# Kernel tuning notes

Hardware: AMD Instinct MI355X
Metric: run time of the kernel (lower is better)

## Reference

```python
import jax, jax.numpy as jnp
import numpy as np
from jax import lax

NUM_GROUP = 512    # G: number of FPS centers
GROUP_SIZE = 32    # M: KNN neighbors per center


def setup_inputs() -> dict:
    key = jax.random.key(0)
    xyz = jax.random.normal(key, (32, 8192, 3), dtype=jnp.float32)  # B N 3
    return {"xyz": xyz}


def _fps(xyz, num_group):
    """Iterative farthest point sampling. xyz: [B,N,3] -> idx [B,G] int32.
    Deterministic start at point 0 (matching pointnet2-style fps)."""
    B, N, _ = xyz.shape

    def step(carry, _):
        dists, last_idx = carry                       # dists: [B,N] running min sq-dist
        last = xyz[jnp.arange(B), last_idx]           # [B,3] most recent center
        d = jnp.sum((xyz - last[:, None, :]) ** 2, axis=-1)  # [B,N]
        dists = jnp.minimum(dists, d)
        nxt = jnp.argmax(dists, axis=-1).astype(jnp.int32)   # farthest point
        return (dists, nxt), nxt

    init_idx = jnp.zeros((B,), jnp.int32)
    init_d = jnp.full((B, N), jnp.inf, xyz.dtype)
    (_, _), idxs = lax.scan(step, (init_d, init_idx), None, length=num_group - 1)
    return jnp.concatenate([init_idx[None, :], idxs], axis=0).T  # [B,G]


def reference(xyz):
    B, N, _ = xyz.shape
    G, M = NUM_GROUP, GROUP_SIZE

    fps_idx = _fps(xyz, G)                              # [B,G] int32
    center = xyz[jnp.arange(B)[:, None], fps_idx]       # [B,G,3]

    # KNN: for each center, k nearest points in xyz (squared euclidean)
    # dist2[b,g,n] = |c|^2 + |x|^2 - 2 c.x   -> [B,G,N]
    x2 = jnp.sum(xyz * xyz, axis=-1)                    # [B,N]
    c2 = jnp.sum(center * center, axis=-1)              # [B,G]
    dist2 = c2[:, :, None] + x2[:, None, :] - 2.0 * jnp.einsum('bgd,bnd->bgn', center, xyz)
    _, idx = lax.top_k(-dist2, M)                       # [B,G,M] nearest-first

    neighborhood = xyz[jnp.arange(B)[:, None, None], idx]   # [B,G,M,3]
    neighborhood = neighborhood - center[:, :, None, :]
    return neighborhood, center, fps_idx
```

## Files before the change

kernel.cpp:

```cpp
#include <hip/hip_runtime.h>
#include <math.h>

#define BATCH  32
#define NPTS   8192
#define NGROUP 512
#define MSIZE  32

#define FPS_THREADS 512
#define SXYZ_FLOATS (NPTS * 3)
#define DYN_LDS_BYTES (SXYZ_FLOATS * 4)

#define NBLOCKS      256
#define WORKER_BLKS  (NBLOCKS - BATCH)
#define WORKER_WAVES (WORKER_BLKS * 8)
#define WPB          (WORKER_WAVES / BATCH)
#define PROG_STRIDE  16

typedef float v2f __attribute__((ext_vector_type(2)));

template<int CTRL>
__device__ __forceinline__ float dpp_max_f32(float x) {
    int o = __builtin_amdgcn_update_dpp(0, __float_as_int(x), CTRL, 0xF, 0xF, true);
    float f = __int_as_float(o);
    return x > f ? x : f;
}
template<int CTRL>
__device__ __forceinline__ unsigned dpp_min_u32_full(unsigned x) {
    unsigned o = (unsigned)__builtin_amdgcn_update_dpp(0, (int)x, CTRL, 0xF, 0xF, true);
    return o < x ? o : x;
}

__device__ __forceinline__ void fps_body(const float* __restrict__ xyz,
                                         float* __restrict__ out_center,
                                         float* __restrict__ out_fps,
                                         unsigned* __restrict__ prog,
                                         float* sxyz)
{
#pragma clang fp contract(off)
    __shared__ unsigned long long gkey[3];

    const int b    = blockIdx.x;
    const int t    = threadIdx.x;
    const int lane = t & 63;
    const float* bp = xyz + (size_t)b * NPTS * 3;
    const float4* bp4 = reinterpret_cast<const float4*>(bp);
    float4* s4 = reinterpret_cast<float4*>(sxyz);

    v2f px2[8], py2[8], pz2[8], dist2[8];
    {
        float f[48];
        #pragma unroll
        for (int q = 0; q < 12; ++q) {
            float4 v = bp4[t * 12 + q];
            s4[t * 12 + q] = v;
            f[q*4+0] = v.x; f[q*4+1] = v.y; f[q*4+2] = v.z; f[q*4+3] = v.w;
        }
        #pragma unroll
        for (int j = 0; j < 8; ++j) {
            px2[j] = (v2f){f[6*j+0], f[6*j+3]};
            py2[j] = (v2f){f[6*j+1], f[6*j+4]};
            pz2[j] = (v2f){f[6*j+2], f[6*j+5]};
            dist2[j] = (v2f){INFINITY, INFINITY};
        }
    }
    if (t == 0) { gkey[0] = 0; gkey[1] = 0; gkey[2] = 0; }
    __syncthreads();

    if (t == 0) {
        out_fps[(size_t)b * NGROUP] = 0.0f;
        __hip_atomic_store(&out_center[(size_t)(b*NGROUP)*3 + 0], sxyz[0],
                           __ATOMIC_RELAXED, __HIP_MEMORY_SCOPE_AGENT);
        __hip_atomic_store(&out_center[(size_t)(b*NGROUP)*3 + 1], sxyz[1],
                           __ATOMIC_RELAXED, __HIP_MEMORY_SCOPE_AGENT);
        __hip_atomic_store(&out_center[(size_t)(b*NGROUP)*3 + 2], sxyz[2],
                           __ATOMIC_RELAXED, __HIP_MEMORY_SCOPE_AGENT);
    }

    int last = 0;
    for (int g = 1; g < NGROUP; ++g) {
        const int slot = g % 3;
        const int nxt  = (g + 1) % 3;
        float lx = sxyz[last*3 + 0];
        float ly = sxyz[last*3 + 1];
        float lz = sxyz[last*3 + 2];

        #pragma unroll
        for (int j = 0; j < 8; ++j) {
            v2f dx = px2[j] - lx;
            v2f dy = py2[j] - ly;
            v2f dz = pz2[j] - lz;
            v2f t1 = dx * dx;
            v2f t2 = dy * dy;
            v2f t3 = dz * dz;
            v2f s  = t1 + t2;
            v2f d  = s + t3;
            dist2[j] = __builtin_elementwise_min(dist2[j], d);
        }
        v2f mm0 = __builtin_elementwise_max(dist2[0], dist2[1]);
        v2f mm1 = __builtin_elementwise_max(dist2[2], dist2[3]);
        v2f mm2 = __builtin_elementwise_max(dist2[4], dist2[5]);
        v2f mm3 = __builtin_elementwise_max(dist2[6], dist2[7]);
        v2f mma = __builtin_elementwise_max(mm0, mm1);
        v2f mmb = __builtin_elementwise_max(mm2, mm3);
        v2f mmc = __builtin_elementwise_max(mma, mmb);
        float m_t = fmaxf(mmc.x, mmc.y);

        float m = m_t;
        m = dpp_max_f32<0xB1>(m);
        m = dpp_max_f32<0x4E>(m);
        m = dpp_max_f32<0x141>(m);
        m = dpp_max_f32<0x140>(m);
        m = dpp_max_f32<0x142>(m);
        m = dpp_max_f32<0x143>(m);
        float wmax = __int_as_float(__builtin_amdgcn_readlane(__float_as_int(m), 63));

        unsigned long long mask = __ballot(m_t == wmax);
        int l = __ffsll((long long)mask) - 1;

        unsigned lj = 0;
        #pragma unroll
        for (int j = 15; j >= 0; --j) {
            float dj = (j & 1) ? dist2[j >> 1].y : dist2[j >> 1].x;
            lj = (dj == wmax) ? (unsigned)j : lj;
        }
        unsigned idx = ((unsigned)t << 4) | lj;
        unsigned widx = (unsigned)__builtin_amdgcn_readlane((int)idx, l);

        if (lane == 63) {
            unsigned long long key =
                (((unsigned long long)__float_as_uint(wmax)) << 32) | (unsigned)~widx;
            atomicMax(&gkey[slot], key);
            if (t == 63) gkey[nxt] = 0;
        }
        __syncthreads();

        unsigned long long kq = gkey[slot];
        int fi = (int)(~(unsigned)kq);
        last = fi;
        if (t == 0) {
            out_fps[(size_t)b * NGROUP + g] = (float)fi;
            const size_t o3 = ((size_t)(b * NGROUP + g)) * 3;
            __hip_atomic_store(&out_center[o3 + 0], sxyz[fi*3 + 0],
                               __ATOMIC_RELAXED, __HIP_MEMORY_SCOPE_AGENT);
            __hip_atomic_store(&out_center[o3 + 1], sxyz[fi*3 + 1],
                               __ATOMIC_RELAXED, __HIP_MEMORY_SCOPE_AGENT);
            __hip_atomic_store(&out_center[o3 + 2], sxyz[fi*3 + 2],
                               __ATOMIC_RELAXED, __HIP_MEMORY_SCOPE_AGENT);
            if ((g & 7) == 7)
                __hip_atomic_store(&prog[b * PROG_STRIDE], (unsigned)(g + 1),
                                   __ATOMIC_RELEASE, __HIP_MEMORY_SCOPE_AGENT);
        }
    }
}

__device__ __forceinline__ void knn_one_group(const float* __restrict__ bp,
                                              const float4* __restrict__ bp4,
                                              int gid, int lane,
                                              float cx, float cy, float cz,
                                              float* __restrict__ out_nbhd)
{
    unsigned kl[4];
    #pragma unroll
    for (int k = 0; k < 4; ++k) kl[k] = 0xFFFFFFFFu;

    for (int c = 0; c < 32; ++c) {
        int f4 = c * 192 + lane * 3;
        float4 a  = bp4[f4+0];
        float4 bq = bp4[f4+1];
        float4 cq = bp4[f4+2];
        unsigned p0 = (unsigned)(c * 256 + lane * 4);
        v2f xA = (v2f){a.x,  a.w},  yA = (v2f){a.y,  bq.x}, zA = (v2f){a.z,  bq.y};
        v2f xB = (v2f){bq.z, cq.y}, yB = (v2f){bq.w, cq.z}, zB = (v2f){cq.x, cq.w};
        v2f dxA = xA - cx, dyA = yA - cy, dzA = zA - cz;
        v2f dxB = xB - cx, dyB = yB - cy, dzB = zB - cz;
        v2f dA = dxA*dxA + dyA*dyA + dzA*dzA;
        v2f dB = dxB*dxB + dyB*dyB + dzB*dzB;
        float ds[4] = {dA.x, dA.y, dB.x, dB.y};
        #pragma unroll
        for (int k = 0; k < 4; ++k) {
            unsigned key = (__float_as_uint(ds[k]) & 0xFFFFE000u) | (p0 + k);
            if (key < kl[3]) {
                kl[3] = key;
                #pragma unroll
                for (int q = 3; q > 0; --q) {
                    if (kl[q] < kl[q-1]) {
                        unsigned tk = kl[q]; kl[q] = kl[q-1]; kl[q-1] = tk;
                    }
                }
            }
        }
    }

    int keep = 0;
    #pragma unroll 1
    for (int r = 0; r < MSIZE; ++r) {
        unsigned k = kl[0];
        k = dpp_min_u32_full<0xB1>(k);
        k = dpp_min_u32_full<0x4E>(k);
        k = dpp_min_u32_full<0x141>(k);
        k = dpp_min_u32_full<0x140>(k);
        {
            unsigned o = __shfl_xor(k, 16);
            k = o < k ? o : k;
            o = __shfl_xor(k, 32);
            k = o < k ? o : k;
        }
        if (lane == r) keep = (int)(k & 0x1FFFu);
        if (kl[0] == k) {
            kl[0] = kl[1]; kl[1] = kl[2]; kl[2] = kl[3];
            kl[3] = 0xFFFFFFFFu;
        }
    }

    if (lane < MSIZE) {
        size_t o = ((size_t)gid * MSIZE + lane) * 3;
        float x = bp[keep*3+0], y = bp[keep*3+1], z = bp[keep*3+2];
        out_nbhd[o+0] = x - cx;
        out_nbhd[o+1] = y - cy;
        out_nbhd[o+2] = z - cz;
    }
}

__global__ __launch_bounds__(FPS_THREADS, 2)
void fused_kernel(const float* __restrict__ xyz,
                  float* __restrict__ out_center,
                  float* __restrict__ out_fps,
                  float* __restrict__ out_nbhd,
                  unsigned* __restrict__ prog)
{
    extern __shared__ float sxyz[];

    if (blockIdx.x < BATCH) {
        fps_body(xyz, out_center, out_fps, prog, sxyz);
        return;
    }

    const int t    = threadIdx.x;
    const int lane = t & 63;
    const int wid  = t >> 6;
    const int ww   = (blockIdx.x - BATCH) * 8 + wid;
    const int b    = ww & 31;
    const int g0   = ww >> 5;
    const float* bp = xyz + (size_t)b * NPTS * 3;
    const float4* bp4 = reinterpret_cast<const float4*>(bp);

    for (int g = g0; g < NGROUP; g += WPB) {
        while ((int)__hip_atomic_load(&prog[b * PROG_STRIDE],
                                      __ATOMIC_ACQUIRE, __HIP_MEMORY_SCOPE_AGENT) <= g)
            __builtin_amdgcn_s_sleep(8);

        const int gid = b * NGROUP + g;
        float cx = __hip_atomic_load(&out_center[(size_t)gid*3+0],
                                     __ATOMIC_RELAXED, __HIP_MEMORY_SCOPE_AGENT);
        float cy = __hip_atomic_load(&out_center[(size_t)gid*3+1],
                                     __ATOMIC_RELAXED, __HIP_MEMORY_SCOPE_AGENT);
        float cz = __hip_atomic_load(&out_center[(size_t)gid*3+2],
                                     __ATOMIC_RELAXED, __HIP_MEMORY_SCOPE_AGENT);
        knn_one_group(bp, bp4, gid, lane, cx, cy, cz, out_nbhd);
    }
}

__global__ __launch_bounds__(FPS_THREADS, 2)
void fps_kernel(const float* __restrict__ xyz,
                float* __restrict__ out_center,
                float* __restrict__ out_fps)
{
#pragma clang fp contract(off)
    extern __shared__ float sxyz[];
    __shared__ unsigned long long gkey[3];

    const int b    = blockIdx.x;
    const int t    = threadIdx.x;
    const int lane = t & 63;
    const float* bp = xyz + (size_t)b * NPTS * 3;
    const float4* bp4 = reinterpret_cast<const float4*>(bp);
    float4* s4 = reinterpret_cast<float4*>(sxyz);

    v2f px2[8], py2[8], pz2[8], dist2[8];
    {
        float f[48];
        #pragma unroll
        for (int q = 0; q < 12; ++q) {
            float4 v = bp4[t * 12 + q];
            s4[t * 12 + q] = v;
            f[q*4+0] = v.x; f[q*4+1] = v.y; f[q*4+2] = v.z; f[q*4+3] = v.w;
        }
        #pragma unroll
        for (int j = 0; j < 8; ++j) {
            px2[j] = (v2f){f[6*j+0], f[6*j+3]};
            py2[j] = (v2f){f[6*j+1], f[6*j+4]};
            pz2[j] = (v2f){f[6*j+2], f[6*j+5]};
            dist2[j] = (v2f){INFINITY, INFINITY};
        }
    }
    if (t == 0) { gkey[0] = 0; gkey[1] = 0; gkey[2] = 0; }
    __syncthreads();

    if (t == 0) {
        out_fps[(size_t)b * NGROUP] = 0.0f;
        out_center[(size_t)(b * NGROUP) * 3 + 0] = sxyz[0];
        out_center[(size_t)(b * NGROUP) * 3 + 1] = sxyz[1];
        out_center[(size_t)(b * NGROUP) * 3 + 2] = sxyz[2];
    }

    int last = 0;
    for (int g = 1; g < NGROUP; ++g) {
        const int slot = g % 3;
        const int nxt  = (g + 1) % 3;
        float lx = sxyz[last*3 + 0];
        float ly = sxyz[last*3 + 1];
        float lz = sxyz[last*3 + 2];

        #pragma unroll
        for (int j = 0; j < 8; ++j) {
            v2f dx = px2[j] - lx;
            v2f dy = py2[j] - ly;
            v2f dz = pz2[j] - lz;
            v2f t1 = dx * dx;
            v2f t2 = dy * dy;
            v2f t3 = dz * dz;
            v2f s  = t1 + t2;
            v2f d  = s + t3;
            dist2[j] = __builtin_elementwise_min(dist2[j], d);
        }
        v2f mm0 = __builtin_elementwise_max(dist2[0], dist2[1]);
        v2f mm1 = __builtin_elementwise_max(dist2[2], dist2[3]);
        v2f mm2 = __builtin_elementwise_max(dist2[4], dist2[5]);
        v2f mm3 = __builtin_elementwise_max(dist2[6], dist2[7]);
        v2f mma = __builtin_elementwise_max(mm0, mm1);
        v2f mmb = __builtin_elementwise_max(mm2, mm3);
        v2f mmc = __builtin_elementwise_max(mma, mmb);
        float m_t = fmaxf(mmc.x, mmc.y);

        float m = m_t;
        m = dpp_max_f32<0xB1>(m);
        m = dpp_max_f32<0x4E>(m);
        m = dpp_max_f32<0x141>(m);
        m = dpp_max_f32<0x140>(m);
        m = dpp_max_f32<0x142>(m);
        m = dpp_max_f32<0x143>(m);
        float wmax = __int_as_float(__builtin_amdgcn_readlane(__float_as_int(m), 63));

        unsigned long long mask = __ballot(m_t == wmax);
        int l = __ffsll((long long)mask) - 1;

        unsigned lj = 0;
        #pragma unroll
        for (int j = 15; j >= 0; --j) {
            float dj = (j & 1) ? dist2[j >> 1].y : dist2[j >> 1].x;
            lj = (dj == wmax) ? (unsigned)j : lj;
        }
        unsigned idx = ((unsigned)t << 4) | lj;
        unsigned widx = (unsigned)__builtin_amdgcn_readlane((int)idx, l);

        if (lane == 63) {
            unsigned long long key =
                (((unsigned long long)__float_as_uint(wmax)) << 32) | (unsigned)~widx;
            atomicMax(&gkey[slot], key);
            if (t == 63) gkey[nxt] = 0;
        }
        __syncthreads();

        unsigned long long kq = gkey[slot];
        int fi = (int)(~(unsigned)kq);
        last = fi;
        if (t == 0) {
            out_fps[(size_t)b * NGROUP + g] = (float)fi;
            out_center[((size_t)(b * NGROUP + g)) * 3 + 0] = sxyz[fi*3 + 0];
            out_center[((size_t)(b * NGROUP + g)) * 3 + 1] = sxyz[fi*3 + 1];
            out_center[((size_t)(b * NGROUP + g)) * 3 + 2] = sxyz[fi*3 + 2];
        }
    }
}

__global__ __launch_bounds__(256)
void knn_kernel(const float* __restrict__ xyz,
                const float* __restrict__ center,
                float* __restrict__ out_nbhd)
{
    const int lane = threadIdx.x & 63;
    const int gid  = blockIdx.x * 4 + (threadIdx.x >> 6);
    const int b    = gid >> 9;
    const float* bp = xyz + (size_t)b * NPTS * 3;
    const float4* bp4 = reinterpret_cast<const float4*>(bp);
    const float cx = center[(size_t)gid*3+0];
    const float cy = center[(size_t)gid*3+1];
    const float cz = center[(size_t)gid*3+2];
    knn_one_group(bp, bp4, gid, lane, cx, cy, cz, out_nbhd);
}

extern "C" void kernel_launch(void* const* d_in, const int* in_sizes, int n_in,
                              void* d_out, int out_size, void* d_ws, size_t ws_size,
                              hipStream_t stream)
{
    const float* xyz = (const float*)d_in[0];
    float* out        = (float*)d_out;
    float* out_nbhd   = out;
    float* out_center = out + (size_t)BATCH*NGROUP*MSIZE*3;
    float* out_fps    = out_center + (size_t)BATCH*NGROUP*3;

    hipFuncSetAttribute(reinterpret_cast<const void*>(fused_kernel),
                        hipFuncAttributeMaxDynamicSharedMemorySize,
                        DYN_LDS_BYTES);
    hipFuncSetAttribute(reinterpret_cast<const void*>(fps_kernel),
                        hipFuncAttributeMaxDynamicSharedMemorySize,
                        DYN_LDS_BYTES);

    bool fused_ok = false;
    if (d_ws != nullptr && ws_size >= (size_t)BATCH * PROG_STRIDE * sizeof(unsigned)) {
        unsigned* prog = (unsigned*)d_ws;
        hipMemsetAsync(prog, 0, (size_t)BATCH * PROG_STRIDE * sizeof(unsigned), stream);

        const float* a_xyz = xyz;
        float* a_oc = out_center; float* a_of = out_fps; float* a_on = out_nbhd;
        unsigned* a_pr = prog;
        void* args[5] = {(void*)&a_xyz, (void*)&a_oc, (void*)&a_of,
                         (void*)&a_on, (void*)&a_pr};
        hipError_t e = hipLaunchCooperativeKernel(
            reinterpret_cast<const void*>(fused_kernel),
            dim3(NBLOCKS), dim3(FPS_THREADS), args, DYN_LDS_BYTES, stream);
        fused_ok = (e == hipSuccess);
    }

    if (!fused_ok) {
        fps_kernel<<<dim3(BATCH), dim3(FPS_THREADS), DYN_LDS_BYTES, stream>>>(xyz, out_center, out_fps);
        knn_kernel<<<dim3(BATCH*NGROUP/4), dim3(256), 0, stream>>>(xyz, out_center, out_nbhd);
    }
}
```

Measured before the change: 602.8 us.

## Batch FPS center stores into chunks and relax worker polling

```diff
diff --git a/kernel.cpp b/kernel.cpp
--- a/kernel.cpp
+++ b/kernel.cpp
@@ -15,6 +15,7 @@
 #define WORKER_WAVES (WORKER_BLKS * 8)
 #define WPB          (WORKER_WAVES / BATCH)
 #define PROG_STRIDE  16
+#define CHUNK        64
 
 typedef float v2f __attribute__((ext_vector_type(2)));
 
@@ -38,6 +39,7 @@
 {
 #pragma clang fp contract(off)
     __shared__ unsigned long long gkey[3];
+    __shared__ int s_fi[NGROUP];
 
     const int b    = blockIdx.x;
     const int t    = threadIdx.x;
@@ -63,18 +65,10 @@
             dist2[j] = (v2f){INFINITY, INFINITY};
         }
     }
-    if (t == 0) { gkey[0] = 0; gkey[1] = 0; gkey[2] = 0; }
+    if (t == 0) { gkey[0] = 0; gkey[1] = 0; gkey[2] = 0; s_fi[0] = 0; }
     __syncthreads();
 
-    if (t == 0) {
-        out_fps[(size_t)b * NGROUP] = 0.0f;
-        __hip_atomic_store(&out_center[(size_t)(b*NGROUP)*3 + 0], sxyz[0],
-                           __ATOMIC_RELAXED, __HIP_MEMORY_SCOPE_AGENT);
-        __hip_atomic_store(&out_center[(size_t)(b*NGROUP)*3 + 1], sxyz[1],
-                           __ATOMIC_RELAXED, __HIP_MEMORY_SCOPE_AGENT);
-        __hip_atomic_store(&out_center[(size_t)(b*NGROUP)*3 + 2], sxyz[2],
-                           __ATOMIC_RELAXED, __HIP_MEMORY_SCOPE_AGENT);
-    }
+    if (t == 0) out_fps[(size_t)b * NGROUP] = 0.0f;
 
     int last = 0;
     for (int g = 1; g < NGROUP; ++g) {
@@ -139,18 +133,38 @@
         last = fi;
         if (t == 0) {
             out_fps[(size_t)b * NGROUP + g] = (float)fi;
-            const size_t o3 = ((size_t)(b * NGROUP + g)) * 3;
-            __hip_atomic_store(&out_center[o3 + 0], sxyz[fi*3 + 0],
-                               __ATOMIC_RELAXED, __HIP_MEMORY_SCOPE_AGENT);
-            __hip_atomic_store(&out_center[o3 + 1], sxyz[fi*3 + 1],
-                               __ATOMIC_RELAXED, __HIP_MEMORY_SCOPE_AGENT);
-            __hip_atomic_store(&out_center[o3 + 2], sxyz[fi*3 + 2],
-                               __ATOMIC_RELAXED, __HIP_MEMORY_SCOPE_AGENT);
-            if ((g & 7) == 7)
-                __hip_atomic_store(&prog[b * PROG_STRIDE], (unsigned)(g + 1),
+            s_fi[g] = fi;
+        }
+
+        if ((g & (CHUNK - 1)) == 0) {
+            if (t < 3 * CHUNK) {
+                const int gi = (g - CHUNK) + t / 3;
+                const int c  = t % 3;
+                const int f2 = s_fi[gi];
+                __hip_atomic_store(&out_center[((size_t)(b * NGROUP + gi)) * 3 + c],
+                                   sxyz[f2*3 + c],
+                                   __ATOMIC_RELAXED, __HIP_MEMORY_SCOPE_AGENT);
+            }
+        } else if ((g & (CHUNK - 1)) == 1 && g > 1) {
+            if (t == 0)
+                __hip_atomic_store(&prog[b * PROG_STRIDE], (unsigned)(g - 1),
                                    __ATOMIC_RELEASE, __HIP_MEMORY_SCOPE_AGENT);
         }
     }
+
+    __syncthreads();
+    if (t < 3 * CHUNK) {
+        const int gi = NGROUP - CHUNK + t / 3;
+        const int c  = t % 3;
+        const int f2 = s_fi[gi];
+        __hip_atomic_store(&out_center[((size_t)(b * NGROUP + gi)) * 3 + c],
+                           sxyz[f2*3 + c],
+                           __ATOMIC_RELAXED, __HIP_MEMORY_SCOPE_AGENT);
+    }
+    __syncthreads();
+    if (t == 0)
+        __hip_atomic_store(&prog[b * PROG_STRIDE], (unsigned)NGROUP,
+                           __ATOMIC_RELEASE, __HIP_MEMORY_SCOPE_AGENT);
 }
 
 __device__ __forceinline__ void knn_one_group(const float* __restrict__ bp,
@@ -246,8 +260,10 @@
 
     for (int g = g0; g < NGROUP; g += WPB) {
         while ((int)__hip_atomic_load(&prog[b * PROG_STRIDE],
-                                      __ATOMIC_ACQUIRE, __HIP_MEMORY_SCOPE_AGENT) <= g)
-            __builtin_amdgcn_s_sleep(8);
+                                      __ATOMIC_RELAXED, __HIP_MEMORY_SCOPE_AGENT) <= g)
+            __builtin_amdgcn_s_sleep(32);
+        (void)__hip_atomic_load(&prog[b * PROG_STRIDE],
+                                __ATOMIC_ACQUIRE, __HIP_MEMORY_SCOPE_AGENT);
 
         const int gid = b * NGROUP + g;
         float cx = __hip_atomic_load(&out_center[(size_t)gid*3+0],
```

After: 603.6 us. About the same (+0.1%).
